# Kernel optimization log

Hardware: AMD Instinct MI355X
Metric: run time of the kernel (lower is better)

The kernel has to match this reference:

```python
import jax, jax.numpy as jnp
import numpy as np

N_P, E_P = 50000, 400000
N_L, E_L = 50000, 400000
B = 256  # number of graphs per side
NEG_GAT = 0.2   # GATv2 leaky-relu slope
NEG_FC = 0.01   # nn.LeakyReLU default slope


def _gatv2(x, ei, Wl, Wr, att, b, H, C):
    """GATv2Conv (concat heads, add_self_loops=True). Wl/Wr: [in, H*C], att: [H, C], b: [H*C]."""
    N = x.shape[0]
    sl = jnp.arange(N)
    src = jnp.concatenate([ei[0], sl])
    dst = jnp.concatenate([ei[1], sl])
    xl = (x @ Wl).reshape(N, H, C)   # source transform (messages)
    xr = (x @ Wr).reshape(N, H, C)   # target transform
    e = jax.nn.leaky_relu(xl[src] + xr[dst], NEG_GAT)          # [E+N, H, C]
    logits = jnp.einsum('ehc,hc->eh', e, att)                   # [E+N, H]
    m = jax.ops.segment_max(logits, dst, num_segments=N)        # segment softmax
    a = jnp.exp(logits - m[dst])
    alpha = a / jax.ops.segment_sum(a, dst, num_segments=N)[dst]
    out = jax.ops.segment_sum(xl[src] * alpha[..., None], dst, num_segments=N)
    return out.reshape(N, H * C) + b


def _mean_pool(x, batch, nb):
    s = jax.ops.segment_sum(x, batch, num_segments=nb)
    c = jax.ops.segment_sum(jnp.ones((x.shape[0],), x.dtype), batch, num_segments=nb)
    return s / jnp.maximum(c, 1.0)[:, None]


def setup_inputs() -> dict:
    key = jax.random.key(0)
    ks = jax.random.split(key, 48)
    i = [0]
    def nrm(shape, fan_in):
        k = ks[i[0]]; i[0] += 1
        return jax.random.normal(k, shape, jnp.float32) / np.sqrt(fan_in)
    inp = {}
    inp['protein_x'] = jax.random.normal(ks[40], (N_P, 10), jnp.float32)
    inp['ligand_x'] = jax.random.normal(ks[41], (N_L, 5), jnp.float32)
    inp['protein_edge_index'] = jax.random.randint(ks[42], (2, E_P), 0, N_P)
    inp['ligand_edge_index'] = jax.random.randint(ks[43], (2, E_L), 0, N_L)
    inp['protein_batch'] = (jnp.arange(N_P) * B) // N_P  # sorted graph ids, all segments nonempty
    inp['ligand_batch'] = (jnp.arange(N_L) * B) // N_L
    # GATv2 params: layer1 heads=2 out=128, layer2 heads=1 out=256
    inp['p1_Wl'] = nrm((10, 256), 10); inp['p1_Wr'] = nrm((10, 256), 10)
    inp['p1_att'] = nrm((2, 128), 128); inp['p1_b'] = jnp.zeros((256,), jnp.float32)
    inp['p2_Wl'] = nrm((256, 256), 256); inp['p2_Wr'] = nrm((256, 256), 256)
    inp['p2_att'] = nrm((1, 256), 256); inp['p2_b'] = jnp.zeros((256,), jnp.float32)
    inp['l1_Wl'] = nrm((5, 256), 5); inp['l1_Wr'] = nrm((5, 256), 5)
    inp['l1_att'] = nrm((2, 128), 128); inp['l1_b'] = jnp.zeros((256,), jnp.float32)
    inp['l2_Wl'] = nrm((256, 256), 256); inp['l2_Wr'] = nrm((256, 256), 256)
    inp['l2_att'] = nrm((1, 256), 256); inp['l2_b'] = jnp.zeros((256,), jnp.float32)
    # MultiheadAttention(256, 4) params ([in, out] convention)
    inp['Wq'] = nrm((256, 256), 256); inp['bq'] = jnp.zeros((256,), jnp.float32)
    inp['Wk'] = nrm((256, 256), 256); inp['bk'] = jnp.zeros((256,), jnp.float32)
    inp['Wv'] = nrm((256, 256), 256); inp['bv'] = jnp.zeros((256,), jnp.float32)
    inp['Wo'] = nrm((256, 256), 256); inp['bo'] = jnp.zeros((256,), jnp.float32)
    # fc head
    inp['fc1_w'] = nrm((512, 256), 512); inp['fc1_b'] = jnp.zeros((256,), jnp.float32)
    inp['ln_g'] = jnp.ones((256,), jnp.float32); inp['ln_b'] = jnp.zeros((256,), jnp.float32)
    inp['fc2_w'] = nrm((256, 1), 256); inp['fc2_b'] = jnp.zeros((1,), jnp.float32)
    return inp


def reference(protein_x, protein_edge_index, protein_batch,
              ligand_x, ligand_edge_index, ligand_batch,
              p1_Wl, p1_Wr, p1_att, p1_b, p2_Wl, p2_Wr, p2_att, p2_b,
              l1_Wl, l1_Wr, l1_att, l1_b, l2_Wl, l2_Wr, l2_att, l2_b,
              Wq, bq, Wk, bk, Wv, bv, Wo, bo,
              fc1_w, fc1_b, ln_g, ln_b, fc2_w, fc2_b):
    px = _gatv2(protein_x, protein_edge_index, p1_Wl, p1_Wr, p1_att, p1_b, 2, 128)
    px = _gatv2(px, protein_edge_index, p2_Wl, p2_Wr, p2_att, p2_b, 1, 256)
    px = _mean_pool(px, protein_batch, B)                        # [B, 256]
    lx = _gatv2(ligand_x, ligand_edge_index, l1_Wl, l1_Wr, l1_att, l1_b, 2, 128)
    lx = _gatv2(lx, ligand_edge_index, l2_Wl, l2_Wr, l2_att, l2_b, 1, 256)
    lx = _mean_pool(lx, ligand_batch, B)                         # [B, 256]
    # cross attention with q/k/v seq length 1
    D, H = 256, 4
    d = D // H
    qh = (px @ Wq + bq).reshape(B, H, d)
    kh = (lx @ Wk + bk).reshape(B, H, d)
    vh = (lx @ Wv + bv).reshape(B, H, d)
    scores = (qh * kh).sum(-1) / jnp.sqrt(jnp.float32(d))        # [B, H], 1 key
    w = jax.nn.softmax(scores[..., None], axis=-1)               # all ones (single key)
    attn = (w * vh).reshape(B, D) @ Wo + bo                      # [B, 256]
    comb = jnp.concatenate([px, attn], axis=1)                   # [B, 512]
    h = comb @ fc1_w + fc1_b
    mu = h.mean(-1, keepdims=True)
    var = h.var(-1, keepdims=True)
    h = (h - mu) / jnp.sqrt(var + 1e-5) * ln_g + ln_b
    h = jax.nn.leaky_relu(h, NEG_FC)
    return h @ fc2_w + fc2_b                                     # [B, 1]
```

## Files before the change

kernel.cpp:

```cpp
#include <hip/hip_runtime.h>
#include <math.h>

typedef unsigned short u16;
typedef __attribute__((ext_vector_type(8))) short bf16x8;
typedef __attribute__((ext_vector_type(4))) float f32x4;

#define LOG2E 1.4426950408889634f

__device__ inline u16 f2bf(float x) {
  unsigned int u = __float_as_uint(x);
  u += 0x7fffu + ((u >> 16) & 1u);
  return (u16)(u >> 16);
}
__device__ inline float bf2f(u16 h) {
  return __uint_as_float(((unsigned int)h) << 16);
}
__device__ inline float4 ld_bf4(const u16* p) {
  ushort4 v = *(const ushort4*)p;
  return make_float4(bf2f(v.x), bf2f(v.y), bf2f(v.z), bf2f(v.w));
}
__device__ inline void gload_lds16(const u16* g, char* lds) {
  __builtin_amdgcn_global_load_lds(
      (const __attribute__((address_space(1))) unsigned int*)g,
      (__attribute__((address_space(3))) unsigned int*)lds, 16, 0, 0);
}

__global__ void k_setup(int* __restrict__ cnt, int nz,
                        const float* __restrict__ W2pl, const float* __restrict__ W2pr,
                        const float* __restrict__ W2ll, const float* __restrict__ W2lr,
                        u16* __restrict__ Whp, u16* __restrict__ Wlp,
                        u16* __restrict__ Whl, u16* __restrict__ Wll_o,
                        const float* __restrict__ xp, int Kp, int Np,
                        const float* __restrict__ xl_, int Kl, int Nl,
                        const float* __restrict__ W1pl, const float* __restrict__ W1pr,
                        const float* __restrict__ W1ll, const float* __restrict__ W1lr,
                        u16* __restrict__ xlh_p, u16* __restrict__ xrh_p,
                        u16* __restrict__ xlh_l, u16* __restrict__ xrh_l,
                        int linPer,
                        const float* __restrict__ Wo, const float* __restrict__ fc1w_,
                        float* __restrict__ Wof) {
  __shared__ float xs[16][8];
  __shared__ float sW[256];
  const int zb = (nz + 255) / 256;
  if ((int)blockIdx.x < zb) {
    int i = blockIdx.x * 256 + threadIdx.x;
    if (i < nz) cnt[i] = 0;
    return;
  }
  int wb = blockIdx.x - zb;
  if (wb < 1024) {
    int n = wb & 511;
    int side = wb >> 9;
    int col = n & 255;
    int k = threadIdx.x;
    const float* W = side == 0 ? (n < 256 ? W2pl : W2pr) : (n < 256 ? W2ll : W2lr);
    float w = W[k * 256 + col];
    u16* Wh = side ? Whl : Whp;
    u16* Wlo = side ? Wll_o : Wlp;
    u16 hb = f2bf(w);
    Wh[n * 256 + k] = hb;
    Wlo[n * 256 + k] = f2bf(w - bf2f(hb));
    return;
  }
  int wb2 = wb - 1024;
  if (wb2 >= 2 * linPer) {
    int row = wb2 - 2 * linPer;
    if (row >= 256) return;
    int jj = threadIdx.x;
    sW[jj] = Wo[row * 256 + jj];
    __syncthreads();
    float a0 = 0.f, a1 = 0.f, a2 = 0.f, a3 = 0.f;
    for (int c = 0; c < 256; c += 4) {
      a0 = fmaf(sW[c], fc1w_[(256 + c) * 256 + jj], a0);
      a1 = fmaf(sW[c + 1], fc1w_[(256 + c + 1) * 256 + jj], a1);
      a2 = fmaf(sW[c + 2], fc1w_[(256 + c + 2) * 256 + jj], a2);
      a3 = fmaf(sW[c + 3], fc1w_[(256 + c + 3) * 256 + jj], a3);
    }
    Wof[row * 256 + jj] = (a0 + a1) + (a2 + a3);
    return;
  }
  const int side = wb2 / linPer;
  const float* x = side ? xl_ : xp;
  const int K = side ? Kl : Kp;
  const int N = side ? Nl : Np;
  const float* Wl = side ? W1ll : W1pl;
  const float* Wr = side ? W1lr : W1pr;
  u16* xlh = side ? xlh_l : xlh_p;
  u16* xrh = side ? xrh_l : xrh_p;
  int base = (wb2 - side * linPer) * 8;
  if (base >= N) return;
  int j = threadIdx.x;
  int tot = 8 * K;
  for (int i = j; i < tot; i += 256) {
    int r = i / K, k = i - r * K;
    if (base + r < N) xs[k][r] = x[(size_t)(base + r) * K + k];
  }
  __syncthreads();
  float al[8] = {}, ar[8] = {};
  for (int k = 0; k < K; ++k) {
    float wl = Wl[k * 256 + j];
    float wr = Wr[k * 256 + j];
#pragma unroll
    for (int r = 0; r < 8; ++r) {
      al[r] = fmaf(xs[k][r], wl, al[r]);
      ar[r] = fmaf(xs[k][r], wr, ar[r]);
    }
  }
#pragma unroll
  for (int r = 0; r < 8; ++r) {
    int n = base + r;
    if (n < N) {
      xlh[(size_t)n * 256 + j] = f2bf(al[r]);
      xrh[(size_t)n * 256 + j] = f2bf(ar[r]);
    }
  }
}

__global__ void k_histb(const int* __restrict__ eip, int Ep, const int* __restrict__ eil,
                        int El, int* __restrict__ cntp, int* __restrict__ cntl,
                        int histB,
                        const float* __restrict__ Wv, const float* __restrict__ Wof,
                        const float* __restrict__ fc1w_, const float* __restrict__ bv,
                        const float* __restrict__ bo, const float* __restrict__ fc1b,
                        float* __restrict__ W2, float* __restrict__ biasEff) {
  __shared__ float sV[256];
  if ((int)blockIdx.x >= histB) {
    int g2 = blockIdx.x - histB;
    int jj = threadIdx.x;
    if (g2 < 256) {
      sV[jj] = Wv[g2 * 256 + jj];
      __syncthreads();
      float a0 = 0.f, a1 = 0.f, a2 = 0.f, a3 = 0.f;
      for (int m = 0; m < 256; m += 4) {
        a0 = fmaf(sV[m], Wof[m * 256 + jj], a0);
        a1 = fmaf(sV[m + 1], Wof[(m + 1) * 256 + jj], a1);
        a2 = fmaf(sV[m + 2], Wof[(m + 2) * 256 + jj], a2);
        a3 = fmaf(sV[m + 3], Wof[(m + 3) * 256 + jj], a3);
      }
      W2[g2 * 256 + jj] = (a0 + a1) + (a2 + a3);
    } else {
      float acc = fc1b[jj];
      for (int k = 0; k < 256; ++k) acc = fmaf(bv[k], Wof[k * 256 + jj], acc);
      for (int k = 0; k < 256; ++k) acc = fmaf(bo[k], fc1w_[(256 + k) * 256 + jj], acc);
      biasEff[jj] = acc;
    }
    return;
  }
  int e = blockIdx.x * blockDim.x + threadIdx.x;
  if (e < Ep) atomicAdd(&cntp[eip[Ep + e]], 1);
  else if (e < Ep + El) { int e2 = e - Ep; atomicAdd(&cntl[eil[El + e2]], 1); }
}

__global__ void k_scan1b(const int* __restrict__ cntp, int Np, const int* __restrict__ cntl,
                         int Nl, int nbp, int* __restrict__ offsp, int* __restrict__ offsl,
                         int* __restrict__ curp, int* __restrict__ curl,
                         int* __restrict__ bsum) {
  __shared__ int s[256];
  int tid = threadIdx.x;
  int side = ((int)blockIdx.x >= nbp) ? 1 : 0;
  int blk = side ? (blockIdx.x - nbp) : blockIdx.x;
  const int* cnt = side ? cntl : cntp;
  int* offs = side ? offsl : offsp;
  int* cur = side ? curl : curp;
  int N = side ? Nl : Np;
  int i = blk * 256 + tid;
  int v = (i < N) ? cnt[i] : 0;
  if (i < N) cur[i] = 0;
  s[tid] = v;
  __syncthreads();
  for (int off = 1; off < 256; off <<= 1) {
    int t = 0;
    if (tid >= off) t = s[tid - off];
    __syncthreads();
    if (tid >= off) s[tid] += t;
    __syncthreads();
  }
  if (i < N) offs[i] = s[tid] - v;
  if (tid == 255) bsum[side * 256 + blk] = s[255];
}

__global__ void k_scan2b(int* __restrict__ bsum, int nbp, int nbl) {
  __shared__ int s[256];
  int side = blockIdx.x;
  int nb = side ? nbl : nbp;
  int* bs = bsum + side * 256;
  int tid = threadIdx.x;
  int v = (tid < nb) ? bs[tid] : 0;
  s[tid] = v;
  __syncthreads();
  for (int off = 1; off < 256; off <<= 1) {
    int t = 0;
    if (tid >= off) t = s[tid - off];
    __syncthreads();
    if (tid >= off) s[tid] += t;
    __syncthreads();
  }
  if (tid < nb) bs[tid] = s[tid] - v;
}

__global__ void k_fillb(const int* __restrict__ eip, int Ep, const int* __restrict__ eil,
                        int El, const int* __restrict__ offsp, const int* __restrict__ offsl,
                        const int* __restrict__ bsum,
                        int* __restrict__ curp, int* __restrict__ curl,
                        int* __restrict__ csrp, int* __restrict__ csrl) {
  int e = blockIdx.x * blockDim.x + threadIdx.x;
  if (e < Ep) {
    int d = eip[Ep + e];
    int pos = offsp[d] + bsum[d >> 8] + atomicAdd(&curp[d], 1);
    csrp[pos] = eip[e];
  } else if (e < Ep + El) {
    int e2 = e - Ep;
    int d = eil[El + e2];
    int pos = offsl[d] + bsum[256 + (d >> 8)] + atomicAdd(&curl[d], 1);
    csrl[pos] = eil[e2];
  }
}

__global__ void __launch_bounds__(256, 2) k_mm_dual_b(
    const u16* __restrict__ A_p, const u16* __restrict__ A_l,
    const u16* __restrict__ Bh_p, const u16* __restrict__ Bl_p,
    const u16* __restrict__ Bh_l, const u16* __restrict__ Bl_l,
    u16* __restrict__ XLh_p, u16* __restrict__ XRh_p,
    u16* __restrict__ XLh_l, u16* __restrict__ XRh_l, int Np, int Nl, int Rp, int Rtot) {
  __shared__ __align__(16) char smem[49152];
  const int gid = blockIdx.x;
  const int rblk = (gid >> 5) * 8 + (gid & 7);
  const int col = (gid >> 3) & 3;
  if (rblk >= Rtot) return;
  const int side = (rblk >= Rp) ? 1 : 0;
  const int rloc = side ? rblk - Rp : rblk;
  const u16* A = side ? A_l : A_p;
  const u16* Bhi = side ? Bh_l : Bh_p;
  const u16* Blo = side ? Bl_l : Bl_p;
  u16* XLh = side ? XLh_l : XLh_p;
  u16* XRh = side ? XRh_l : XRh_p;
  const int M = side ? Nl : Np;
  const int t = threadIdx.x;
  const int rowBase = rloc * 128;
  const int j0 = col * 128;
  const int lane = t & 63;
  const int wid = t >> 6;
  const int srow0 = wid * 32 + (lane >> 2);
  const int cL = lane & 3;
  int rA0 = rowBase + srow0;
  if (rA0 >= M) rA0 = M - 1;
  int rA1 = rowBase + srow0 + 16;
  if (rA1 >= M) rA1 = M - 1;
  const int rB0 = j0 + srow0;
  const int rB1 = j0 + srow0 + 16;
  const int c0 = (cL - ((srow0 >> 1) & 3)) & 3;
  const int c1 = (cL - (((srow0 + 16) >> 1) & 3)) & 3;
  const size_t gA0 = (size_t)rA0 * 256 + c0 * 8;
  const size_t gA1 = (size_t)rA1 * 256 + c1 * 8;
  const size_t gB0 = (size_t)rB0 * 256 + c0 * 8;
  const size_t gB1 = (size_t)rB1 * 256 + c1 * 8;
  const int seg = wid * 2048;
  const int wm = (wid & 1) * 64;
  const int wn = (wid >> 1) * 64;
  const int kq = lane >> 4;
  const int mr = lane & 15;
  int offA[4], offB[4];
#pragma unroll
  for (int i = 0; i < 4; ++i) {
    int m = wm + i * 16 + mr;
    offA[i] = m * 64 + ((kq + (m >> 1)) & 3) * 16;
    int n = wn + i * 16 + mr;
    offB[i] = n * 64 + ((kq + (n >> 1)) & 3) * 16;
  }
  f32x4 acc[4][4] = {};
  auto stage = [&](int bsel, int kt) {
    char* bb = smem + bsel * 24576;
    const int k0 = kt * 32;
    gload_lds16(A + gA0 + k0, bb + seg);
    gload_lds16(A + gA1 + k0, bb + seg + 1024);
    gload_lds16(Bhi + gB0 + k0, bb + 8192 + seg);
    gload_lds16(Bhi + gB1 + k0, bb + 8192 + seg + 1024);
    gload_lds16(Blo + gB0 + k0, bb + 16384 + seg);
    gload_lds16(Blo + gB1 + k0, bb + 16384 + seg + 1024);
  };
  stage(0, 0);
#pragma unroll
  for (int kt = 0; kt < 8; ++kt) {
    const int cur = kt & 1;
    asm volatile("s_waitcnt vmcnt(0)" ::: "memory");
    __syncthreads();
    if (kt < 7) stage(cur ^ 1, kt + 1);
    const char* bb = smem + cur * 24576;
    bf16x8 a[4], bh[4], bl[4];
#pragma unroll
    for (int i = 0; i < 4; ++i) {
      a[i] = *(const bf16x8*)(bb + offA[i]);
      bh[i] = *(const bf16x8*)(bb + 8192 + offB[i]);
      bl[i] = *(const bf16x8*)(bb + 16384 + offB[i]);
    }
#pragma unroll
    for (int i = 0; i < 4; ++i)
#pragma unroll
      for (int j = 0; j < 4; ++j) {
        acc[i][j] = __builtin_amdgcn_mfma_f32_16x16x32_bf16(a[i], bh[j], acc[i][j], 0, 0, 0);
        acc[i][j] = __builtin_amdgcn_mfma_f32_16x16x32_bf16(a[i], bl[j], acc[i][j], 0, 0, 0);
      }
  }
  __syncthreads();
  u16* wtile = (u16*)(smem + wid * 8192);
#pragma unroll
  for (int i = 0; i < 4; ++i)
#pragma unroll
    for (int j = 0; j < 4; ++j)
#pragma unroll
      for (int r = 0; r < 4; ++r)
        wtile[(i * 16 + kq * 4 + r) * 64 + j * 16 + mr] = f2bf(acc[i][j][r]);
  u16* cbase = (col < 2) ? XLh : XRh;
  const int cb = (col < 2) ? j0 : j0 - 256;
  const int r8 = lane >> 3;
  const int c8 = lane & 7;
#pragma unroll
  for (int rr = 0; rr < 8; ++rr) {
    int lr = rr * 8 + r8;
    uint4 v = *(const uint4*)&wtile[lr * 64 + c8 * 8];
    int row = rowBase + wm + lr;
    if (row < M) *(uint4*)&cbase[(size_t)row * 256 + cb + wn + c8 * 8] = v;
  }
}

#define GAT_DOT(a, q)                                                          \
  {                                                                            \
    float t0 = a.x + rd.x, t1 = a.y + rd.y, t2 = a.z + rd.z, t3 = a.w + rd.w;  \
    q = fmaf(t3, wa6.w, fabsf(t3) * wa4.w);                                    \
    q = fmaf(fabsf(t2), wa4.z, fmaf(t2, wa6.z, q));                            \
    q = fmaf(fabsf(t1), wa4.y, fmaf(t1, wa6.y, q));                            \
    q = fmaf(fabsf(t0), wa4.x, fmaf(t0, wa6.x, q));                            \
  }

template <int H>
__global__ void k_gat_gather_b(
    const u16* __restrict__ xlh_p, const u16* __restrict__ xrh_p, u16* __restrict__ out_p,
    const u16* __restrict__ xlh_l, const u16* __restrict__ xrh_l, u16* __restrict__ out_l,
    const int* __restrict__ csr_p, const int* __restrict__ offs_p,
    const int* __restrict__ cnt_p,
    const int* __restrict__ csr_l, const int* __restrict__ offs_l,
    const int* __restrict__ cnt_l, const int* __restrict__ bsum,
    const float* __restrict__ att_p, const float* __restrict__ bias_p,
    const float* __restrict__ att_l, const float* __restrict__ bias_l,
    int Np, int Nl) {
  const int side = blockIdx.y;
  const u16* xlh = side ? xlh_l : xlh_p;
  const u16* xrh = side ? xrh_l : xrh_p;
  u16* out = side ? out_l : out_p;
  const int* csr = side ? csr_l : csr_p;
  const int* offs = side ? offs_l : offs_p;
  const int* cnt = side ? cnt_l : cnt_p;
  const float* att = side ? att_l : att_p;
  const float* bias = side ? bias_l : bias_p;
  const int N = side ? Nl : Np;
  int d = blockIdx.x * 4 + (threadIdx.x >> 6);
  if (d >= N) return;
  const int lo4 = (threadIdx.x & 63) * 4;
  const float4 rd = ld_bf4(&xrh[(size_t)d * 256 + lo4]);
  const float4 wa = *(const float4*)&att[lo4];
  const float4 wa6 = make_float4(0.6f * LOG2E * wa.x, 0.6f * LOG2E * wa.y,
                                 0.6f * LOG2E * wa.z, 0.6f * LOG2E * wa.w);
  const float4 wa4 = make_float4(0.4f * LOG2E * wa.x, 0.4f * LOG2E * wa.y,
                                 0.4f * LOG2E * wa.z, 0.4f * LOG2E * wa.w);
  const float4 xd = ld_bf4(&xlh[(size_t)d * 256 + lo4]);
  float base;
  GAT_DOT(xd, base)
#pragma unroll
  for (int off = 1; off <= (H == 2 ? 16 : 32); off <<= 1) base += __shfl_xor(base, off, 64);
  float l0 = 1.f, l1 = 0.f, l2 = 0.f, l3 = 0.f;
  float4 acc0 = xd;
  float4 acc1 = make_float4(0.f, 0.f, 0.f, 0.f);
  float4 acc2 = make_float4(0.f, 0.f, 0.f, 0.f);
  float4 acc3 = make_float4(0.f, 0.f, 0.f, 0.f);
  const int o0 = offs[d] + bsum[side * 256 + (d >> 8)];
  const int c = cnt[d];
  int j = 0;
  for (; j + 3 < c; j += 4) {
    int s0 = csr[o0 + j], s1 = csr[o0 + j + 1], s2 = csr[o0 + j + 2], s3 = csr[o0 + j + 3];
    float4 a0 = ld_bf4(&xlh[(size_t)s0 * 256 + lo4]);
    float4 a1 = ld_bf4(&xlh[(size_t)s1 * 256 + lo4]);
    float4 a2 = ld_bf4(&xlh[(size_t)s2 * 256 + lo4]);
    float4 a3 = ld_bf4(&xlh[(size_t)s3 * 256 + lo4]);
    float q0, q1, q2, q3;
    GAT_DOT(a0, q0)
    GAT_DOT(a1, q1)
    GAT_DOT(a2, q2)
    GAT_DOT(a3, q3)
#pragma unroll
    for (int off = 1; off <= (H == 2 ? 16 : 32); off <<= 1) {
      q0 += __shfl_xor(q0, off, 64);
      q1 += __shfl_xor(q1, off, 64);
      q2 += __shfl_xor(q2, off, 64);
      q3 += __shfl_xor(q3, off, 64);
    }
    float w0 = __builtin_amdgcn_exp2f(q0 - base), w1 = __builtin_amdgcn_exp2f(q1 - base);
    float w2 = __builtin_amdgcn_exp2f(q2 - base), w3 = __builtin_amdgcn_exp2f(q3 - base);
    l0 += w0; l1 += w1; l2 += w2; l3 += w3;
    acc0.x = fmaf(w0, a0.x, acc0.x); acc0.y = fmaf(w0, a0.y, acc0.y);
    acc0.z = fmaf(w0, a0.z, acc0.z); acc0.w = fmaf(w0, a0.w, acc0.w);
    acc1.x = fmaf(w1, a1.x, acc1.x); acc1.y = fmaf(w1, a1.y, acc1.y);
    acc1.z = fmaf(w1, a1.z, acc1.z); acc1.w = fmaf(w1, a1.w, acc1.w);
    acc2.x = fmaf(w2, a2.x, acc2.x); acc2.y = fmaf(w2, a2.y, acc2.y);
    acc2.z = fmaf(w2, a2.z, acc2.z); acc2.w = fmaf(w2, a2.w, acc2.w);
    acc3.x = fmaf(w3, a3.x, acc3.x); acc3.y = fmaf(w3, a3.y, acc3.y);
    acc3.z = fmaf(w3, a3.z, acc3.z); acc3.w = fmaf(w3, a3.w, acc3.w);
  }
  for (; j < c; ++j) {
    int s0 = csr[o0 + j];
    float4 a0 = ld_bf4(&xlh[(size_t)s0 * 256 + lo4]);
    float q0;
    GAT_DOT(a0, q0)
#pragma unroll
    for (int off = 1; off <= (H == 2 ? 16 : 32); off <<= 1) q0 += __shfl_xor(q0, off, 64);
    float w0 = __builtin_amdgcn_exp2f(q0 - base);
    l0 += w0;
    acc0.x = fmaf(w0, a0.x, acc0.x); acc0.y = fmaf(w0, a0.y, acc0.y);
    acc0.z = fmaf(w0, a0.z, acc0.z); acc0.w = fmaf(w0, a0.w, acc0.w);
  }
  float inv = 1.f / (l0 + l1 + l2 + l3);
  float ax = acc0.x + acc1.x + acc2.x + acc3.x;
  float ay = acc0.y + acc1.y + acc2.y + acc3.y;
  float az = acc0.z + acc1.z + acc2.z + acc3.z;
  float aw = acc0.w + acc1.w + acc2.w + acc3.w;
  const float4 b4 = *(const float4*)&bias[lo4];
  ushort4 hv;
  hv.x = f2bf(ax * inv + b4.x);
  hv.y = f2bf(ay * inv + b4.y);
  hv.z = f2bf(az * inv + b4.z);
  hv.w = f2bf(aw * inv + b4.w);
  *(ushort4*)&out[(size_t)d * 256 + lo4] = hv;
}

#define POOL_C 8
__global__ void k_pool_part(const u16* __restrict__ xp, const int* __restrict__ bp, int Np,
                            const u16* __restrict__ xl_, const int* __restrict__ bl_, int Nl,
                            float* __restrict__ PPpart, float* __restrict__ LPpart) {
  const int b = blockIdx.x;
  const int side = blockIdx.y;
  const int chunk = blockIdx.z;
  const u16* x = side ? xl_ : xp;
  const int* batch = side ? bl_ : bp;
  const int N = side ? Nl : Np;
  float* part = side ? LPpart : PPpart;
  int t = threadIdx.x;
  __shared__ int sss, sse;
  __shared__ float red[4][256];
  if (t == 0) {
    int lo = 0, hi = N;
    while (lo < hi) { int mid = (lo + hi) >> 1; if (batch[mid] < b) lo = mid + 1; else hi = mid; }
    sss = lo;
    lo = 0; hi = N;
    while (lo < hi) { int mid = (lo + hi) >> 1; if (batch[mid] < b + 1) lo = mid + 1; else hi = mid; }
    sse = lo;
  }
  __syncthreads();
  int len = sse - sss;
  int per = (len + POOL_C - 1) / POOL_C;
  int st = sss + chunk * per;
  int en = st + per;
  if (en > sse) en = sse;
  const int r = t >> 6;
  const int lane = t & 63;
  float4 acc = make_float4(0.f, 0.f, 0.f, 0.f);
  for (int n = st + r; n < en; n += 4) {
    float4 v = ld_bf4(&x[(size_t)n * 256 + lane * 4]);
    acc.x += v.x; acc.y += v.y; acc.z += v.z; acc.w += v.w;
  }
  red[r][lane * 4 + 0] = acc.x;
  red[r][lane * 4 + 1] = acc.y;
  red[r][lane * 4 + 2] = acc.z;
  red[r][lane * 4 + 3] = acc.w;
  __syncthreads();
  part[((size_t)chunk * 256 + b) * 256 + t] =
      red[0][t] + red[1][t] + red[2][t] + red[3][t];
}

__global__ void k_head(const float* __restrict__ PPpart, const float* __restrict__ LPpart,
                       const int* __restrict__ bp, int Np,
                       const int* __restrict__ bl_, int Nl,
                       const float* __restrict__ fc1w, const float* __restrict__ W2,
                       const float* __restrict__ biasEff,
                       const float* __restrict__ lng, const float* __restrict__ lnb,
                       const float* __restrict__ fc2w, const float* __restrict__ fc2b,
                       float* __restrict__ out) {
  int b = blockIdx.x;
  int t = threadIdx.x;
  int j = t & 255;
  __shared__ float xs0[256], xs1[256];
  __shared__ float part[2][256];
  __shared__ float r1[256], r2[256];
  __shared__ float smu, srs;
  __shared__ int seg[4];
  if (t < 2) {
    const int* batch = t ? bl_ : bp;
    int N = t ? Nl : Np;
    int lo = 0, hi = N;
    while (lo < hi) { int mid = (lo + hi) >> 1; if (batch[mid] < b) lo = mid + 1; else hi = mid; }
    seg[t * 2] = lo;
    lo = 0; hi = N;
    while (lo < hi) { int mid = (lo + hi) >> 1; if (batch[mid] < b + 1) lo = mid + 1; else hi = mid; }
    seg[t * 2 + 1] = lo;
  }
  __syncthreads();
  if (t < 256) {
    float accp = 0.f;
#pragma unroll
    for (int c = 0; c < POOL_C; ++c) accp += PPpart[((size_t)c * 256 + b) * 256 + j];
    xs0[j] = accp / fmaxf((float)(seg[1] - seg[0]), 1.f);
  } else {
    float accl = 0.f;
#pragma unroll
    for (int c = 0; c < POOL_C; ++c) accl += LPpart[((size_t)c * 256 + b) * 256 + j];
    xs1[j] = accl / fmaxf((float)(seg[3] - seg[2]), 1.f);
  }
  __syncthreads();
  {
    const float* src = (t < 256) ? xs0 : xs1;
    const float* W = (t < 256) ? fc1w : W2;
    float a0 = 0.f, a1 = 0.f, a2 = 0.f, a3 = 0.f;
    for (int k = 0; k < 256; k += 4) {
      a0 = fmaf(src[k], W[k * 256 + j], a0);
      a1 = fmaf(src[k + 1], W[(k + 1) * 256 + j], a1);
      a2 = fmaf(src[k + 2], W[(k + 2) * 256 + j], a2);
      a3 = fmaf(src[k + 3], W[(k + 3) * 256 + j], a3);
    }
    part[t >> 8][j] = (a0 + a1) + (a2 + a3);
  }
  __syncthreads();
  float h = 0.f;
  if (t < 256) {
    h = part[0][j] + part[1][j] + biasEff[j];
    r1[j] = h;
    r2[j] = h * h;
  }
  __syncthreads();
  for (int off = 128; off > 0; off >>= 1) {
    if (t < off) { r1[t] += r1[t + off]; r2[t] += r2[t + off]; }
    __syncthreads();
  }
  if (t == 0) {
    float mu = r1[0] / 256.f;
    float var = r2[0] / 256.f - mu * mu;
    smu = mu;
    srs = 1.f / sqrtf(var + 1e-5f);
  }
  __syncthreads();
  if (t < 256) {
    float hn = (h - smu) * srs * lng[j] + lnb[j];
    hn = hn > 0.f ? hn : 0.01f * hn;
    r1[j] = hn * fc2w[j];
  }
  __syncthreads();
  for (int off = 128; off > 0; off >>= 1) {
    if (t < off) r1[t] += r1[t + off];
    __syncthreads();
  }
  if (t == 0) out[b] = r1[0] + fc2b[0];
}

extern "C" void kernel_launch(void* const* d_in, const int* in_sizes, int n_in,
                              void* d_out, int out_size, void* d_ws, size_t ws_size,
                              hipStream_t stream) {
  const float* px = (const float*)d_in[0];
  const float* lx = (const float*)d_in[1];
  const int* pei = (const int*)d_in[2];
  const int* lei = (const int*)d_in[3];
  const int* pb = (const int*)d_in[4];
  const int* lb = (const int*)d_in[5];
  const float* p1_Wl = (const float*)d_in[6];
  const float* p1_Wr = (const float*)d_in[7];
  const float* p1_att = (const float*)d_in[8];
  const float* p1_b = (const float*)d_in[9];
  const float* p2_Wl = (const float*)d_in[10];
  const float* p2_Wr = (const float*)d_in[11];
  const float* p2_att = (const float*)d_in[12];
  const float* p2_b = (const float*)d_in[13];
  const float* l1_Wl = (const float*)d_in[14];
  const float* l1_Wr = (const float*)d_in[15];
  const float* l1_att = (const float*)d_in[16];
  const float* l1_b = (const float*)d_in[17];
  const float* l2_Wl = (const float*)d_in[18];
  const float* l2_Wr = (const float*)d_in[19];
  const float* l2_att = (const float*)d_in[20];
  const float* l2_b = (const float*)d_in[21];
  const float* Wv = (const float*)d_in[26];
  const float* bv = (const float*)d_in[27];
  const float* Wo = (const float*)d_in[28];
  const float* bo = (const float*)d_in[29];
  const float* fc1w = (const float*)d_in[30];
  const float* fc1b = (const float*)d_in[31];
  const float* lng = (const float*)d_in[32];
  const float* lnb = (const float*)d_in[33];
  const float* fc2w = (const float*)d_in[34];
  const float* fc2b = (const float*)d_in[35];

  const int NPn = in_sizes[4];
  const int NLn = in_sizes[5];
  const int EPe = in_sizes[2] / 2;
  const int ELe = in_sizes[3] / 2;
  const int KP = in_sizes[0] / NPn;
  const int KL = in_sizes[1] / NLn;

  const int Nmax = NPn > NLn ? NPn : NLn;
  const int Emax = EPe > ELe ? EPe : ELe;
  size_t NF = (size_t)Nmax * 256;

  u16* XLh_p = (u16*)d_ws;
  u16* XRh_p = XLh_p + NF;
  u16* Ah_p = XRh_p + NF;
  u16* XLh_l = Ah_p + NF;
  u16* XRh_l = XLh_l + NF;
  u16* Ah_l = XRh_l + NF;
  u16* Wth = Ah_l + NF;
  u16* Wtl = Wth + 2 * 512 * 256;
  float* PPpart = (float*)(Wtl + 2 * 512 * 256);
  float* LPpart = PPpart + (size_t)POOL_C * 256 * 256;
  int* cnt = (int*)(LPpart + (size_t)POOL_C * 256 * 256);
  int* cur = cnt + 2 * (size_t)Nmax;
  int* offs = cur + 2 * (size_t)Nmax;
  int* bsum = offs + 2 * (size_t)Nmax;
  int* csr = bsum + 512;
  int* cnt_l = cnt + Nmax;
  int* cur_l = cur + Nmax;
  int* offs_l = offs + Nmax;
  int* csr_l = csr + Emax;
  float* Wof = (float*)(csr + 2 * (size_t)Emax);
  float* W2f = Wof + 65536;
  float* bEff = W2f + 65536;

  const int nbp = (NPn + 255) / 256;
  const int nbl = (NLn + 255) / 256;
  const int nz = 2 * Nmax;
  const int zb = (nz + 255) / 256;
  const int linPer = (Nmax + 7) / 8;
  const int histB = (EPe + ELe + 255) / 256;

  k_setup<<<zb + 1024 + 2 * linPer + 256, 256, 0, stream>>>(
      cnt, nz, p2_Wl, p2_Wr, l2_Wl, l2_Wr,
      Wth, Wtl, Wth + 512 * 256, Wtl + 512 * 256,
      px, KP, NPn, lx, KL, NLn, p1_Wl, p1_Wr, l1_Wl, l1_Wr,
      XLh_p, XRh_p, XLh_l, XRh_l, linPer, Wo, fc1w, Wof);
  k_histb<<<histB + 257, 256, 0, stream>>>(pei, EPe, lei, ELe, cnt, cnt_l, histB,
                                           Wv, Wof, fc1w, bv, bo, fc1b, W2f, bEff);
  k_scan1b<<<nbp + nbl, 256, 0, stream>>>(cnt, NPn, cnt_l, NLn, nbp, offs, offs_l,
                                          cur, cur_l, bsum);
  k_scan2b<<<2, 256, 0, stream>>>(bsum, nbp, nbl);
  k_fillb<<<(EPe + ELe + 255) / 256, 256, 0, stream>>>(pei, EPe, lei, ELe, offs, offs_l,
                                                       bsum, cur, cur_l, csr, csr_l);
  k_gat_gather_b<2><<<dim3((Nmax + 3) / 4, 2), 256, 0, stream>>>(
      XLh_p, XRh_p, Ah_p, XLh_l, XRh_l, Ah_l,
      csr, offs, cnt, csr_l, offs_l, cnt_l, bsum,
      p1_att, p1_b, l1_att, l1_b, NPn, NLn);
  {
    const int Rp = (NPn + 127) / 128;
    const int Rl = (NLn + 127) / 128;
    const int Rtot = Rp + Rl;
    k_mm_dual_b<<<32 * ((Rtot + 7) / 8), 256, 0, stream>>>(
        Ah_p, Ah_l, Wth, Wtl, Wth + 512 * 256, Wtl + 512 * 256,
        XLh_p, XRh_p, XLh_l, XRh_l, NPn, NLn, Rp, Rtot);
  }
  k_gat_gather_b<1><<<dim3((Nmax + 3) / 4, 2), 256, 0, stream>>>(
      XLh_p, XRh_p, Ah_p, XLh_l, XRh_l, Ah_l,
      csr, offs, cnt, csr_l, offs_l, cnt_l, bsum,
      p2_att, p2_b, l2_att, l2_b, NPn, NLn);
  k_pool_part<<<dim3(256, 2, POOL_C), 256, 0, stream>>>(Ah_p, pb, NPn, Ah_l, lb, NLn,
                                                        PPpart, LPpart);
  k_head<<<256, 512, 0, stream>>>(PPpart, LPpart, pb, NPn, lb, NLn,
                                  fc1w, W2f, bEff, lng, lnb, fc2w, fc2b,
                                  (float*)d_out);
  (void)n_in; (void)out_size; (void)ws_size;
}
```

Baseline: 503.9 us.

## Fuse mean-pool into second GAT gather via float atomics into per-graph sums

The second GATv2 gather no longer writes its bf16 node output. Each destination node's result is atomically added into a per-graph float sum buffer, which the fill kernel zeroes in extra blocks, and the separate partial-pool kernel is removed. This avoids writing and re-reading a 50k×256 activation array and saves one kernel launch. In exchange it issues many float atomics that contend on 256 graph rows, since consecutive nodes share a graph, and the summation order becomes nondeterministic.

```diff
diff --git a/kernel.cpp b/kernel.cpp
--- a/kernel.cpp
+++ b/kernel.cpp
@@ -202,7 +202,14 @@
                         int El, const int* __restrict__ offsp, const int* __restrict__ offsl,
                         const int* __restrict__ bsum,
                         int* __restrict__ curp, int* __restrict__ curl,
-                        int* __restrict__ csrp, int* __restrict__ csrl) {
+                        int* __restrict__ csrp, int* __restrict__ csrl,
+                        int fillB, float* __restrict__ PPool, float* __restrict__ LPool) {
+  if ((int)blockIdx.x >= fillB) {
+    int z = (blockIdx.x - fillB) * 256 + threadIdx.x;
+    if (z < 65536) PPool[z] = 0.f;
+    else LPool[z - 65536] = 0.f;
+    return;
+  }
   int e = blockIdx.x * blockDim.x + threadIdx.x;
   if (e < Ep) {
     int d = eip[Ep + e];
@@ -332,7 +339,7 @@
     q = fmaf(fabsf(t0), wa4.x, fmaf(t0, wa6.x, q));                            \
   }
 
-template <int H>
+template <int H, bool POOL>
 __global__ void k_gat_gather_b(
     const u16* __restrict__ xlh_p, const u16* __restrict__ xrh_p, u16* __restrict__ out_p,
     const u16* __restrict__ xlh_l, const u16* __restrict__ xrh_l, u16* __restrict__ out_l,
@@ -342,6 +349,8 @@
     const int* __restrict__ cnt_l, const int* __restrict__ bsum,
     const float* __restrict__ att_p, const float* __restrict__ bias_p,
     const float* __restrict__ att_l, const float* __restrict__ bias_l,
+    const int* __restrict__ batch_p, const int* __restrict__ batch_l,
+    float* __restrict__ pool_p, float* __restrict__ pool_l,
     int Np, int Nl) {
   const int side = blockIdx.y;
   const u16* xlh = side ? xlh_l : xlh_p;
@@ -423,59 +432,26 @@
   float az = acc0.z + acc1.z + acc2.z + acc3.z;
   float aw = acc0.w + acc1.w + acc2.w + acc3.w;
   const float4 b4 = *(const float4*)&bias[lo4];
-  ushort4 hv;
-  hv.x = f2bf(ax * inv + b4.x);
-  hv.y = f2bf(ay * inv + b4.y);
-  hv.z = f2bf(az * inv + b4.z);
-  hv.w = f2bf(aw * inv + b4.w);
-  *(ushort4*)&out[(size_t)d * 256 + lo4] = hv;
-}
-
-#define POOL_C 8
-__global__ void k_pool_part(const u16* __restrict__ xp, const int* __restrict__ bp, int Np,
-                            const u16* __restrict__ xl_, const int* __restrict__ bl_, int Nl,
-                            float* __restrict__ PPpart, float* __restrict__ LPpart) {
-  const int b = blockIdx.x;
-  const int side = blockIdx.y;
-  const int chunk = blockIdx.z;
-  const u16* x = side ? xl_ : xp;
-  const int* batch = side ? bl_ : bp;
-  const int N = side ? Nl : Np;
-  float* part = side ? LPpart : PPpart;
-  int t = threadIdx.x;
-  __shared__ int sss, sse;
-  __shared__ float red[4][256];
-  if (t == 0) {
-    int lo = 0, hi = N;
-    while (lo < hi) { int mid = (lo + hi) >> 1; if (batch[mid] < b) lo = mid + 1; else hi = mid; }
-    sss = lo;
-    lo = 0; hi = N;
-    while (lo < hi) { int mid = (lo + hi) >> 1; if (batch[mid] < b + 1) lo = mid + 1; else hi = mid; }
-    sse = lo;
-  }
-  __syncthreads();
-  int len = sse - sss;
-  int per = (len + POOL_C - 1) / POOL_C;
-  int st = sss + chunk * per;
-  int en = st + per;
-  if (en > sse) en = sse;
-  const int r = t >> 6;
-  const int lane = t & 63;
-  float4 acc = make_float4(0.f, 0.f, 0.f, 0.f);
-  for (int n = st + r; n < en; n += 4) {
-    float4 v = ld_bf4(&x[(size_t)n * 256 + lane * 4]);
-    acc.x += v.x; acc.y += v.y; acc.z += v.z; acc.w += v.w;
-  }
-  red[r][lane * 4 + 0] = acc.x;
-  red[r][lane * 4 + 1] = acc.y;
-  red[r][lane * 4 + 2] = acc.z;
-  red[r][lane * 4 + 3] = acc.w;
-  __syncthreads();
-  part[((size_t)chunk * 256 + b) * 256 + t] =
-      red[0][t] + red[1][t] + red[2][t] + red[3][t];
-}
-
-__global__ void k_head(const float* __restrict__ PPpart, const float* __restrict__ LPpart,
+  if constexpr (POOL) {
+    const int* batch = side ? batch_l : batch_p;
+    float* pool = side ? pool_l : pool_p;
+    int b = batch[d];
+    float* pp = pool + (size_t)b * 256 + lo4;
+    atomicAdd(pp + 0, ax * inv + b4.x);
+    atomicAdd(pp + 1, ay * inv + b4.y);
+    atomicAdd(pp + 2, az * inv + b4.z);
+    atomicAdd(pp + 3, aw * inv + b4.w);
+  } else {
+    ushort4 hv;
+    hv.x = f2bf(ax * inv + b4.x);
+    hv.y = f2bf(ay * inv + b4.y);
+    hv.z = f2bf(az * inv + b4.z);
+    hv.w = f2bf(aw * inv + b4.w);
+    *(ushort4*)&out[(size_t)d * 256 + lo4] = hv;
+  }
+}
+
+__global__ void k_head(const float* __restrict__ PPool, const float* __restrict__ LPool,
                        const int* __restrict__ bp, int Np,
                        const int* __restrict__ bl_, int Nl,
                        const float* __restrict__ fc1w, const float* __restrict__ W2,
@@ -503,15 +479,9 @@
   }
   __syncthreads();
   if (t < 256) {
-    float accp = 0.f;
-#pragma unroll
-    for (int c = 0; c < POOL_C; ++c) accp += PPpart[((size_t)c * 256 + b) * 256 + j];
-    xs0[j] = accp / fmaxf((float)(seg[1] - seg[0]), 1.f);
+    xs0[j] = PPool[(size_t)b * 256 + j] / fmaxf((float)(seg[1] - seg[0]), 1.f);
   } else {
-    float accl = 0.f;
-#pragma unroll
-    for (int c = 0; c < POOL_C; ++c) accl += LPpart[((size_t)c * 256 + b) * 256 + j];
-    xs1[j] = accl / fmaxf((float)(seg[3] - seg[2]), 1.f);
+    xs1[j] = LPool[(size_t)b * 256 + j] / fmaxf((float)(seg[3] - seg[2]), 1.f);
   }
   __syncthreads();
   {
@@ -613,9 +583,9 @@
   u16* Ah_l = XRh_l + NF;
   u16* Wth = Ah_l + NF;
   u16* Wtl = Wth + 2 * 512 * 256;
-  float* PPpart = (float*)(Wtl + 2 * 512 * 256);
-  float* LPpart = PPpart + (size_t)POOL_C * 256 * 256;
-  int* cnt = (int*)(LPpart + (size_t)POOL_C * 256 * 256);
+  float* PPool = (float*)(Wtl + 2 * 512 * 256);
+  float* LPool = PPool + 65536;
+  int* cnt = (int*)(LPool + 65536);
   int* cur = cnt + 2 * (size_t)Nmax;
   int* offs = cur + 2 * (size_t)Nmax;
   int* bsum = offs + 2 * (size_t)Nmax;
@@ -634,6 +604,7 @@
   const int zb = (nz + 255) / 256;
   const int linPer = (Nmax + 7) / 8;
   const int histB = (EPe + ELe + 255) / 256;
+  const int fillB = (EPe + ELe + 255) / 256;
 
   k_setup<<<zb + 1024 + 2 * linPer + 256, 256, 0, stream>>>(
       cnt, nz, p2_Wl, p2_Wr, l2_Wl, l2_Wr,
@@ -645,12 +616,13 @@
   k_scan1b<<<nbp + nbl, 256, 0, stream>>>(cnt, NPn, cnt_l, NLn, nbp, offs, offs_l,
                                           cur, cur_l, bsum);
   k_scan2b<<<2, 256, 0, stream>>>(bsum, nbp, nbl);
-  k_fillb<<<(EPe + ELe + 255) / 256, 256, 0, stream>>>(pei, EPe, lei, ELe, offs, offs_l,
-                                                       bsum, cur, cur_l, csr, csr_l);
-  k_gat_gather_b<2><<<dim3((Nmax + 3) / 4, 2), 256, 0, stream>>>(
+  k_fillb<<<fillB + 512, 256, 0, stream>>>(pei, EPe, lei, ELe, offs, offs_l,
+                                           bsum, cur, cur_l, csr, csr_l,
+                                           fillB, PPool, LPool);
+  k_gat_gather_b<2, false><<<dim3((Nmax + 3) / 4, 2), 256, 0, stream>>>(
       XLh_p, XRh_p, Ah_p, XLh_l, XRh_l, Ah_l,
       csr, offs, cnt, csr_l, offs_l, cnt_l, bsum,
-      p1_att, p1_b, l1_att, l1_b, NPn, NLn);
+      p1_att, p1_b, l1_att, l1_b, pb, lb, PPool, LPool, NPn, NLn);
   {
     const int Rp = (NPn + 127) / 128;
     const int Rl = (NLn + 127) / 128;
@@ -659,13 +631,11 @@
         Ah_p, Ah_l, Wth, Wtl, Wth + 512 * 256, Wtl + 512 * 256,
         XLh_p, XRh_p, XLh_l, XRh_l, NPn, NLn, Rp, Rtot);
   }
-  k_gat_gather_b<1><<<dim3((Nmax + 3) / 4, 2), 256, 0, stream>>>(
+  k_gat_gather_b<1, true><<<dim3((Nmax + 3) / 4, 2), 256, 0, stream>>>(
       XLh_p, XRh_p, Ah_p, XLh_l, XRh_l, Ah_l,
       csr, offs, cnt, csr_l, offs_l, cnt_l, bsum,
-      p2_att, p2_b, l2_att, l2_b, NPn, NLn);
-  k_pool_part<<<dim3(256, 2, POOL_C), 256, 0, stream>>>(Ah_p, pb, NPn, Ah_l, lb, NLn,
-                                                        PPpart, LPpart);
-  k_head<<<256, 512, 0, stream>>>(PPpart, LPpart, pb, NPn, lb, NLn,
+      p2_att, p2_b, l2_att, l2_b, pb, lb, PPool, LPool, NPn, NLn);
+  k_head<<<256, 512, 0, stream>>>(PPool, LPool, pb, NPn, lb, NLn,
                                   fc1w, W2f, bEff, lng, lnb, fc2w, fc2b,
                                   (float*)d_out);
   (void)n_in; (void)out_size; (void)ws_size;
```

New measurement: 772.4 us. 53.3% more time.
